# Kernel optimization log

Hardware: AMD Instinct MI355X
Metric: run time of the kernel (lower is better)

## Reference

```python
import jax, jax.numpy as jnp
import numpy as np

jax.config.update("jax_enable_x64", True)

B, T, C = 64, 720, 512


def setup_inputs() -> dict:
    key = jax.random.key(0)
    kx, _ = jax.random.split(key)
    x = jax.random.normal(kx, (B, T, C), dtype=jnp.float32)
    # learnable EMA coefficient (scalar parameter)
    alpha = jnp.asarray(0.3, dtype=jnp.float32)
    return {"x": x, "alpha": alpha}


def reference(x, alpha):
    # x: [B, T, C] float32, alpha: scalar float32
    t = x.shape[1]
    alpha_d = alpha.astype(jnp.float64)
    # powers = flip(arange(t)) = [t-1, t-2, ..., 0], double precision as in torch
    powers = jnp.arange(t - 1, -1, -1, dtype=jnp.float64)  # [T]
    base = jnp.power(1.0 - alpha_d, powers)                # (1-a)^(t-1-i), [T]
    divisor = base
    # weights[0] = base[0]; weights[i>=1] = base[i] * alpha
    weights = base * jnp.where(jnp.arange(t) == 0, 1.0, alpha_d)
    # broadcast to [1, T, 1]; compute in float64 (torch promotes f32*f64 -> f64)
    num = jnp.cumsum(x.astype(jnp.float64) * weights[None, :, None], axis=1)
    ma = (num / divisor[None, :, None]).astype(jnp.float32)  # [B, T, C]
    res = x - ma
    return (res, ma)
```

## Files before the change

### kernel.cpp

```cpp
#include <hip/hip_runtime.h>


constexpr int kB = 64;
constexpr int kT = 720;
constexpr int kC = 512;
constexpr int kJ = 16;
constexpr int kL = 45;
constexpr int kNTHREADS = kB * kJ * kC;

__global__ __launch_bounds__(256) void ema_partials(const float* __restrict__ x,
                                                    const float* __restrict__ alphap,
                                                    float* __restrict__ s) {
    const int tid = blockIdx.x * 256 + threadIdx.x;
    const int c   = tid & (kC - 1);
    const int bj  = tid >> 9;
    const int j   = bj & (kJ - 1);
    const int b   = bj >> 4;
    const float alpha = alphap[0];
    const float beta  = 1.0f - alpha;

    const float* xp = x + (size_t)(b * kT + j * kL) * kC + c;

    float p = ((j == 0) ? 1.0f : alpha) * xp[0];
    #pragma unroll
    for (int i = 1; i < kL; ++i)
        p = fmaf(beta, p, alpha * xp[i * kC]);

    s[tid] = p;
}

__global__ __launch_bounds__(256) void ema_apply(const float* __restrict__ x,
                                                 const float* __restrict__ alphap,
                                                 const float* __restrict__ s,
                                                 float* __restrict__ res,
                                                 float* __restrict__ ma) {
    const int tid = blockIdx.x * 256 + threadIdx.x;
    const int c   = tid & (kC - 1);
    const int bj  = tid >> 9;
    const int j   = bj & (kJ - 1);
    const int b   = bj >> 4;
    const float alpha = alphap[0];
    const float beta  = 1.0f - alpha;
    const float betaL = powf(beta, (float)kL);

    const float* sp = s + (size_t)(b * kJ) * kC + c;
    float E = 0.0f;
    for (int k = 0; k < j; ++k)
        E = fmaf(E, betaL, sp[k * kC]);

    const int base = (b * kT + j * kL) * kC + c;
    const float* xp = x   + (size_t)base;
    float*       rp = res + (size_t)base;
    float*       mp = ma  + (size_t)base;

    float e = E;
    #pragma unroll
    for (int i = 0; i < kL; ++i) {
        const float xv = xp[i * kC];
        const float w  = (j == 0 && i == 0) ? 1.0f : alpha;
        e = fmaf(beta, e, w * xv);
        mp[i * kC] = e;
        rp[i * kC] = xv - e;
    }
}

extern "C" void kernel_launch(void* const* d_in, const int* in_sizes, int n_in,
                              void* d_out, int out_size, void* d_ws, size_t ws_size,
                              hipStream_t stream) {
    const float* x      = (const float*)d_in[0];
    const float* alphap = (const float*)d_in[1];
    float* res = (float*)d_out;
    float* ma  = res + (size_t)kB * kT * kC;
    float* s   = (float*)d_ws;

    const int nblk = kNTHREADS / 256;
    ema_partials<<<nblk, 256, 0, stream>>>(x, alphap, s);
    ema_apply   <<<nblk, 256, 0, stream>>>(x, alphap, s, res, ma);
}
```

Before: 273.2 us.

## Fuse EMA partials and apply kernels with shared-memory chunk carry

Merges the two-pass chunked EMA scan into one kernel where each block covers all 16 time chunks for 32 channels of one batch. Chunk partial sums go through shared memory instead of a global workspace, and each thread keeps its 45 inputs in registers so x is read only once. This removes a second read of x, the workspace traffic and one launch, at the cost of higher register pressure and a block-level barrier.

```diff
diff --git a/kernel.cpp b/kernel.cpp
--- a/kernel.cpp
+++ b/kernel.cpp
@@ -1,66 +1,61 @@
 #include <hip/hip_runtime.h>
 
 
-constexpr int kB = 64;
-constexpr int kT = 720;
-constexpr int kC = 512;
-constexpr int kJ = 16;
-constexpr int kL = 45;
-constexpr int kNTHREADS = kB * kJ * kC;
+constexpr int kB  = 64;
+constexpr int kT  = 720;
+constexpr int kC  = 512;
+constexpr int kJ  = 16;
+constexpr int kL  = 45;
+constexpr int kCT = 32;
+constexpr int kBlockThreads = kJ * kCT;
 
-__global__ __launch_bounds__(256) void ema_partials(const float* __restrict__ x,
-                                                    const float* __restrict__ alphap,
-                                                    float* __restrict__ s) {
-    const int tid = blockIdx.x * 256 + threadIdx.x;
-    const int c   = tid & (kC - 1);
-    const int bj  = tid >> 9;
-    const int j   = bj & (kJ - 1);
-    const int b   = bj >> 4;
+__global__ __launch_bounds__(kBlockThreads) void ema_fused(
+        const float* __restrict__ x,
+        const float* __restrict__ alphap,
+        float* __restrict__ res,
+        float* __restrict__ ma) {
+    const int tid = threadIdx.x;
+    const int cl  = tid & (kCT - 1);
+    const int j   = tid >> 5;
+    const int ct  = blockIdx.x;
+    const int b   = blockIdx.y;
+    const int c   = ct * kCT + cl;
+
     const float alpha = alphap[0];
     const float beta  = 1.0f - alpha;
 
-    const float* xp = x + (size_t)(b * kT + j * kL) * kC + c;
+    const size_t base = (size_t)(b * kT + j * kL) * kC + c;
+    const float* xp = x + base;
 
-    float p = ((j == 0) ? 1.0f : alpha) * xp[0];
+    float xv[kL];
+    #pragma unroll
+    for (int i = 0; i < kL; ++i)
+        xv[i] = xp[(size_t)i * kC];
+
+    float p = ((j == 0) ? 1.0f : alpha) * xv[0];
     #pragma unroll
     for (int i = 1; i < kL; ++i)
-        p = fmaf(beta, p, alpha * xp[i * kC]);
+        p = fmaf(beta, p, alpha * xv[i]);
 
-    s[tid] = p;
-}
+    __shared__ float sl[kJ][kCT + 1];
+    sl[j][cl] = p;
+    __syncthreads();
 
-__global__ __launch_bounds__(256) void ema_apply(const float* __restrict__ x,
-                                                 const float* __restrict__ alphap,
-                                                 const float* __restrict__ s,
-                                                 float* __restrict__ res,
-                                                 float* __restrict__ ma) {
-    const int tid = blockIdx.x * 256 + threadIdx.x;
-    const int c   = tid & (kC - 1);
-    const int bj  = tid >> 9;
-    const int j   = bj & (kJ - 1);
-    const int b   = bj >> 4;
-    const float alpha = alphap[0];
-    const float beta  = 1.0f - alpha;
     const float betaL = powf(beta, (float)kL);
-
-    const float* sp = s + (size_t)(b * kJ) * kC + c;
     float E = 0.0f;
     for (int k = 0; k < j; ++k)
-        E = fmaf(E, betaL, sp[k * kC]);
+        E = fmaf(E, betaL, sl[k][cl]);
 
-    const int base = (b * kT + j * kL) * kC + c;
-    const float* xp = x   + (size_t)base;
-    float*       rp = res + (size_t)base;
-    float*       mp = ma  + (size_t)base;
-
+    float* __restrict__ rp = res + base;
+    float* __restrict__ mp = ma  + base;
     float e = E;
     #pragma unroll
     for (int i = 0; i < kL; ++i) {
-        const float xv = xp[i * kC];
+        const float xi = xv[i];
         const float w  = (j == 0 && i == 0) ? 1.0f : alpha;
-        e = fmaf(beta, e, w * xv);
-        mp[i * kC] = e;
-        rp[i * kC] = xv - e;
+        e = fmaf(beta, e, w * xi);
+        mp[(size_t)i * kC] = e;
+        rp[(size_t)i * kC] = xi - e;
     }
 }
 
@@ -71,9 +66,8 @@
     const float* alphap = (const float*)d_in[1];
     float* res = (float*)d_out;
     float* ma  = res + (size_t)kB * kT * kC;
-    float* s   = (float*)d_ws;
+    (void)d_ws; (void)ws_size;
 
-    const int nblk = kNTHREADS / 256;
-    ema_partials<<<nblk, 256, 0, stream>>>(x, alphap, s);
-    ema_apply   <<<nblk, 256, 0, stream>>>(x, alphap, s, res, ma);
+    dim3 grid(kC / kCT, kB);
+    ema_fused<<<grid, kBlockThreads, 0, stream>>>(x, alphap, res, ma);
 }
```

Measured after the change: 273.2 us. About the same (+0.0%).
